# Performance work log

Measured on AMD Instinct MI355X. Metric: run time of the kernel, lower is better.

Reference implementation:

```python
import jax, jax.numpy as jnp
import numpy as np

N, E, T, D, M, G = 131072, 524288, 4, 128, 256, 4096
VOCAB, GH, L, PASSES = 100, 512, 128, 4


def setup_inputs() -> dict:
    key = jax.random.key(0)
    ks = jax.random.split(key, 20)
    node_types = jax.random.randint(ks[0], (N,), 0, VOCAB)
    edge_src = jax.random.randint(ks[1], (E,), 0, N)
    edge_dst = jax.random.randint(ks[2], (E,), 0, N)
    edge_type = jax.random.randint(ks[3], (E,), 0, T)
    inner = jnp.sort(jax.random.randint(ks[4], (G - 1,), 0, N))
    ptr = jnp.concatenate([jnp.zeros((1,), jnp.int64 if inner.dtype == jnp.int64 else jnp.int32),
                           inner, jnp.full((1,), N, inner.dtype)])
    s = 1.0 / np.sqrt(D)
    emb = jax.random.normal(ks[5], (VOCAB, D), jnp.float32)
    W_msg = jax.random.normal(ks[6], (T, M, D), jnp.float32) * s
    b_msg = jax.random.normal(ks[7], (T, M), jnp.float32) * s
    W_ih = jax.random.normal(ks[8], (3 * D, M), jnp.float32) * (1.0 / np.sqrt(M))
    W_hh = jax.random.normal(ks[9], (3 * D, D), jnp.float32) * s
    b_ih = jax.random.normal(ks[10], (3 * D,), jnp.float32) * s
    b_hh = jax.random.normal(ks[11], (3 * D,), jnp.float32) * s
    W_gate = jax.random.normal(ks[12], (1, D), jnp.float32) * s
    b_gate = jax.random.normal(ks[13], (1,), jnp.float32) * s
    W_n2g = jax.random.normal(ks[14], (GH, D), jnp.float32) * s
    b_n2g = jax.random.normal(ks[15], (GH,), jnp.float32) * s
    W_loc = jax.random.normal(ks[16], (L, GH), jnp.float32) * (1.0 / np.sqrt(GH))
    b_loc = jax.random.normal(ks[17], (L,), jnp.float32) * (1.0 / np.sqrt(GH))
    W_lv = jax.random.normal(ks[18], (L, GH), jnp.float32) * (1.0 / np.sqrt(GH))
    b_lv = jax.random.normal(ks[19], (L,), jnp.float32) * (1.0 / np.sqrt(GH))
    return dict(node_types=node_types, edge_src=edge_src, edge_dst=edge_dst,
                edge_type=edge_type, ptr=ptr, emb=emb, W_msg=W_msg, b_msg=b_msg,
                W_ih=W_ih, W_hh=W_hh, b_ih=b_ih, b_hh=b_hh, W_gate=W_gate,
                b_gate=b_gate, W_n2g=W_n2g, b_n2g=b_n2g, W_loc=W_loc, b_loc=b_loc,
                W_lv=W_lv, b_lv=b_lv)


def _ggnn_pass(h, edge_src, edge_dst, edge_type, W_msg, b_msg, W_ih, W_hh, b_ih, b_hh):
    # per-edge-type linear on all nodes: [T, N, M]
    msgs_all = jnp.einsum('nd,tmd->tnm', h, W_msg) + b_msg[:, None, :]
    # gather the message of the edge's type at its source node: [E, M]
    e_msg = msgs_all[edge_type, edge_src]
    # sparse adjacency matmul == scatter-add of source messages into destinations
    agg = jax.ops.segment_sum(e_msg, edge_dst, num_segments=h.shape[0])
    m = jax.nn.relu(agg)
    # torch GRUCell
    gi = m @ W_ih.T + b_ih      # [N, 3D]
    gh = h @ W_hh.T + b_hh      # [N, 3D]
    d = h.shape[1]
    ir, iz, inn = gi[:, :d], gi[:, d:2 * d], gi[:, 2 * d:]
    hr, hz, hn = gh[:, :d], gh[:, d:2 * d], gh[:, 2 * d:]
    r = jax.nn.sigmoid(ir + hr)
    z = jax.nn.sigmoid(iz + hz)
    n = jnp.tanh(inn + r * hn)
    return (1.0 - z) * n + z * h


def reference(node_types, edge_src, edge_dst, edge_type, ptr, emb, W_msg, b_msg,
              W_ih, W_hh, b_ih, b_hh, W_gate, b_gate, W_n2g, b_n2g,
              W_loc, b_loc, W_lv, b_lv):
    h = emb[node_types]  # [N, D]
    for _ in range(PASSES):
        h = _ggnn_pass(h, edge_src, edge_dst, edge_type,
                       W_msg, b_msg, W_ih, W_hh, b_ih, b_hh)
    # gated segment readout (equivalent to per-graph attn @ h slices)
    gate = jax.nn.sigmoid(h @ W_gate.T + b_gate)        # [N, 1]
    hg = h @ W_n2g.T + b_n2g                            # [N, GH]
    seg = jnp.searchsorted(ptr, jnp.arange(h.shape[0]), side='right') - 1
    h_graph = jax.ops.segment_sum(gate * hg, seg, num_segments=ptr.shape[0] - 1)
    z_loc = h_graph @ W_loc.T + b_loc
    z_logvar = h_graph @ W_lv.T + b_lv
    return (z_loc, z_logvar)
```

## Files before the change

### kernel.cpp

```cpp
#include <hip/hip_runtime.h>
#include <cstdint>
#include <cstddef>

#define NN 131072
#define EE 524288
#define GG 4096
#define NPASS 4

typedef __attribute__((ext_vector_type(4))) float f32x4;
typedef __attribute__((ext_vector_type(8))) short bfrag;

__device__ __forceinline__ unsigned short f2bf(float f) {
  union { float f; unsigned u; } v; v.f = f;
  unsigned r = v.u + 0x7fffu + ((v.u >> 16) & 1u);
  return (unsigned short)(r >> 16);
}
__device__ __forceinline__ float bf2f(unsigned short h) {
  union { unsigned u; float f; } v; v.u = ((unsigned)h) << 16;
  return v.f;
}
__device__ __forceinline__ unsigned pack2(float x, float y) {
  return (unsigned)f2bf(x) | ((unsigned)f2bf(y) << 16);
}
__device__ __forceinline__ float sigm(float x) { return 1.f / (1.f + __expf(-x)); }

__device__ __forceinline__ void cp16(unsigned short* l, const unsigned short* g) {
  __builtin_amdgcn_global_load_lds(
      (const __attribute__((address_space(1))) unsigned int*)g,
      (__attribute__((address_space(3))) unsigned int*)l, 16, 0, 0);
}

__global__ void prep_wb(const float* __restrict__ Wmsg, unsigned short* __restrict__ Wb) {
  int idx = blockIdx.x * 256 + threadIdx.x;
  if (idx >= 256 * 512) return;
  int m = idx >> 9, k = idx & 511;
  int t = k >> 7, d = k & 127;
  Wb[idx] = f2bf(Wmsg[((size_t)t * 256 + m) * 128 + d]);
}

__global__ void prep_wgru(const float* __restrict__ Wih, const float* __restrict__ Whh,
                          unsigned short* __restrict__ Wgru) {
  int idx = blockIdx.x * 256 + threadIdx.x;
  if (idx >= 512 * 384) return;
  int j = idx / 384, kk = idx % 384;
  float v;
  if (kk < 256) v = (j < 384) ? Wih[j * 256 + kk] : 0.f;
  else          v = (j < 256) ? Whh[j * 128 + (kk - 256)]
                   : ((j >= 384) ? Whh[(j - 128) * 128 + (kk - 256)] : 0.f);
  int g = (j < 128) ? 0 : (j < 256) ? 1 : (j < 384) ? 2 : 3;
  int d = j & 127;
  Wgru[(size_t)(4 * d + g) * 384 + kk] = f2bf(v);
}

__global__ void prep_bias(const float* __restrict__ bih, const float* __restrict__ bhh,
                          float* __restrict__ biasg) {
  int j = blockIdx.x * 256 + threadIdx.x;
  if (j >= 512) return;
  float v;
  if (j < 256) v = bih[j] + bhh[j];
  else if (j < 384) v = bih[j];
  else v = bhh[j - 128];
  int g = (j < 128) ? 0 : (j < 256) ? 1 : (j < 384) ? 2 : 3;
  int d = j & 127;
  biasg[4 * d + g] = v;
}

__global__ void compose_k(const float* __restrict__ Wloc, const float* __restrict__ Wlv,
                          const float* __restrict__ Wn2g, float* __restrict__ WcT) {
  int b = blockIdx.x;
  int jl = threadIdx.x >> 7, d = threadIdx.x & 127;
  int j = b * 2 + jl;
  const float* wx = (j < 128) ? Wloc + (size_t)j * 512 : Wlv + (size_t)(j - 128) * 512;
  float acc = 0.f;
  for (int k = 0; k < 512; k++) acc += wx[k] * Wn2g[k * 128 + d];
  WcT[d * 256 + j] = acc;
}

__global__ void cvec_k(const float* __restrict__ Wloc, const float* __restrict__ Wlv,
                       const float* __restrict__ bn2g, float* __restrict__ cvec) {
  int j = threadIdx.x;
  const float* wx = (j < 128) ? Wloc + (size_t)j * 512 : Wlv + (size_t)(j - 128) * 512;
  float a = 0.f;
  for (int k = 0; k < 512; k++) a += wx[k] * bn2g[k];
  cvec[j] = a;
}

__global__ void init_h(const int* __restrict__ nt, const float* __restrict__ emb,
                       unsigned short* __restrict__ H) {
  size_t idx = (size_t)blockIdx.x * 256 + threadIdx.x;
  int n = (int)(idx >> 7), d = (int)(idx & 127);
  H[idx] = f2bf(emb[(size_t)nt[n] * 128 + d]);
}

__global__ void cnt4_k(const int* __restrict__ edst, const int* __restrict__ etype,
                       int* __restrict__ cnti) {
  int e = blockIdx.x * 256 + threadIdx.x;
  if (e >= EE) return;
  atomicAdd(&cnti[edst[e] * 4 + etype[e]], 1);
}

__global__ void degsum_k(const int* __restrict__ cnti, int* __restrict__ deg,
                         float* __restrict__ cnt) {
  int n = blockIdx.x * 256 + threadIdx.x;
  if (n >= NN) return;
  int4 c4 = *(const int4*)&cnti[n * 4];
  deg[n] = c4.x + c4.y + c4.z + c4.w;
  float4 f4 = make_float4((float)c4.x, (float)c4.y, (float)c4.z, (float)c4.w);
  *(float4*)&cnt[n * 4] = f4;
}

__global__ __launch_bounds__(1024) void scan_k(const int* __restrict__ deg,
                                               int* __restrict__ rowptr,
                                               int* __restrict__ cursor) {
  __shared__ int part[1024];
  int t = threadIdx.x;
  int base = t * 128;
  int s = 0;
  for (int i = 0; i < 128; i++) s += deg[base + i];
  part[t] = s;
  __syncthreads();
  for (int off = 1; off < 1024; off <<= 1) {
    int v = (t >= off) ? part[t - off] : 0;
    __syncthreads();
    part[t] += v;
    __syncthreads();
  }
  int run = part[t] - s;
  for (int i = 0; i < 128; i++) {
    rowptr[base + i] = run;
    cursor[base + i] = run;
    run += deg[base + i];
  }
  if (t == 1023) rowptr[NN] = run;
}

__global__ void fill_k(const int* __restrict__ esrc, const int* __restrict__ edst,
                       const int* __restrict__ etype, int* __restrict__ cursor,
                       unsigned* __restrict__ epack) {
  int e = blockIdx.x * 256 + threadIdx.x;
  if (e >= EE) return;
  int pos = atomicAdd(&cursor[edst[e]], 1);
  epack[pos] = ((unsigned)etype[e] << 17) | (unsigned)esrc[e];
}

__global__ __launch_bounds__(256) void agg_k(const int* __restrict__ rowptr,
                                             const unsigned* __restrict__ epack,
                                             const unsigned short* __restrict__ H,
                                             unsigned short* __restrict__ s) {
  int n = blockIdx.x * 4 + (threadIdx.x >> 6);
  int lane = threadIdx.x & 63;
  int beg = rowptr[n], end = rowptr[n + 1];
  const unsigned short* hbase = H + lane * 2;
  float a0 = 0.f, a1 = 0.f, b0 = 0.f, b1 = 0.f;
  float c0 = 0.f, c1 = 0.f, d0 = 0.f, d1 = 0.f;
#define ACCUM(P, HV)                                              \
  {                                                               \
    int t_ = (int)((P) >> 17);                                    \
    float v0_ = bf2f((unsigned short)((HV) & 0xffffu));           \
    float v1_ = bf2f((unsigned short)((HV) >> 16));               \
    if (t_ == 0)      { a0 += v0_; a1 += v1_; }                   \
    else if (t_ == 1) { b0 += v0_; b1 += v1_; }                   \
    else if (t_ == 2) { c0 += v0_; c1 += v1_; }                   \
    else              { d0 += v0_; d1 += v1_; }                   \
  }
  for (int base = beg; base < end; base += 64) {
    int cnt = end - base;
    if (cnt > 64) cnt = 64;
    int mye = base + lane;
    unsigned ep = (mye < end) ? epack[mye] : 0u;
    if (cnt > 0) {
      unsigned p = (unsigned)__shfl((int)ep, 0);
      unsigned hv = *(const unsigned*)&hbase[(size_t)(p & 0x1FFFFu) * 128];
      for (int j = 1; j < cnt; j++) {
        unsigned pn = (unsigned)__shfl((int)ep, j);
        unsigned hvn = *(const unsigned*)&hbase[(size_t)(pn & 0x1FFFFu) * 128];
        ACCUM(p, hv);
        p = pn;
        hv = hvn;
      }
      ACCUM(p, hv);
    }
  }
#undef ACCUM
  unsigned short* srow = s + (size_t)n * 512;
  *(unsigned*)&srow[0 * 128 + lane * 2] = pack2(a0, a1);
  *(unsigned*)&srow[1 * 128 + lane * 2] = pack2(b0, b1);
  *(unsigned*)&srow[2 * 128 + lane * 2] = pack2(c0, c1);
  *(unsigned*)&srow[3 * 128 + lane * 2] = pack2(d0, d1);
}

__global__ __launch_bounds__(256, 4) void msgemm_k(
    unsigned short* __restrict__ s, const float* __restrict__ cnt,
    const unsigned short* __restrict__ Wb, const float* __restrict__ bmsg) {
  __shared__ __align__(16) unsigned short As[2][64 * 32];
  __shared__ __align__(16) unsigned short Bs[2][256 * 32];
  int i0 = blockIdx.x * 64;
  int tid = threadIdx.x, lane = tid & 63, w = tid >> 6;
  int wi = w >> 1, wj = w & 1;
  int q = lane >> 4, r = lane & 15;
  int srow = tid >> 2, scol = (tid & 3) * 8;

  const unsigned short* sP = s + (size_t)(i0 + srow) * 512 + scol;
  const unsigned short* WbP = Wb + (size_t)srow * 512 + scol;

  f32x4 acc[2][8];
#pragma unroll
  for (int a = 0; a < 2; a++)
#pragma unroll
    for (int b = 0; b < 8; b++) acc[a][b] = f32x4{0.f, 0.f, 0.f, 0.f};

  cp16(&As[0][w * 512], sP);
#pragma unroll
  for (int c = 0; c < 4; c++)
    cp16(&Bs[0][c * 2048 + w * 512], WbP + (size_t)(c * 64) * 512);
  __syncthreads();

  for (int ks = 0; ks < 16; ks++) {
    int b = ks & 1;
    if (ks < 15) {
      int nb = b ^ 1;
      cp16(&As[nb][w * 512], sP + (ks + 1) * 32);
#pragma unroll
      for (int c = 0; c < 4; c++)
        cp16(&Bs[nb][c * 2048 + w * 512],
             WbP + (size_t)(c * 64) * 512 + (ks + 1) * 32);
    }
    bfrag af[2];
#pragma unroll
    for (int rt = 0; rt < 2; rt++)
      af[rt] = *(const bfrag*)&As[b][(wi * 32 + rt * 16 + r) * 32 + q * 8];
#pragma unroll
    for (int ct = 0; ct < 8; ct++) {
      bfrag bfr = *(const bfrag*)&Bs[b][(wj * 128 + ct * 16 + r) * 32 + q * 8];
#pragma unroll
      for (int rt = 0; rt < 2; rt++)
        acc[rt][ct] =
            __builtin_amdgcn_mfma_f32_16x16x32_bf16(af[rt], bfr, acc[rt][ct], 0, 0, 0);
    }
    __syncthreads();
  }

#pragma unroll
  for (int ct = 0; ct < 8; ct++) {
    int j = wj * 128 + ct * 16 + r;
    float b0 = bmsg[j], b1 = bmsg[256 + j], b2 = bmsg[512 + j], b3 = bmsg[768 + j];
#pragma unroll
    for (int rt = 0; rt < 2; rt++) {
#pragma unroll
      for (int reg = 0; reg < 4; reg++) {
        int il = wi * 32 + rt * 16 + q * 4 + reg;
        float4 c4 = *(const float4*)&cnt[(size_t)(i0 + il) * 4];
        float v = acc[rt][ct][reg] + c4.x * b0 + c4.y * b1 + c4.z * b2 + c4.w * b3;
        v = v > 0.f ? v : 0.f;
        s[(size_t)(i0 + il) * 512 + j] = f2bf(v);
      }
    }
  }
}

__global__ __launch_bounds__(256, 4) void grugemm_k(
    const unsigned short* __restrict__ m,
    const unsigned short* __restrict__ Hc, unsigned short* __restrict__ Hn,
    const unsigned short* __restrict__ Wgru, const float* __restrict__ biasg) {
  __shared__ __align__(16) unsigned short As[2][64 * 32];
  __shared__ __align__(16) unsigned short Bs[2][256 * 32];
  int bcol = blockIdx.x & 1;
  int i0 = (int)(blockIdx.x >> 1) * 64;
  int tid = threadIdx.x, lane = tid & 63, w = tid >> 6;
  int wi = w >> 1, wj = w & 1;
  int q = lane >> 4, r = lane & 15;
  int srow = tid >> 2, scol = (tid & 3) * 8;

  const unsigned short* mP = m + (size_t)(i0 + srow) * 512 + scol;
  const unsigned short* hP = Hc + (size_t)(i0 + srow) * 128 + scol;
  const unsigned short* WgP = Wgru + (size_t)(bcol * 256 + srow) * 384 + scol;

  f32x4 acc[2][8];
#pragma unroll
  for (int a = 0; a < 2; a++)
#pragma unroll
    for (int b = 0; b < 8; b++) acc[a][b] = f32x4{0.f, 0.f, 0.f, 0.f};

  cp16(&As[0][w * 512], mP);
#pragma unroll
  for (int c = 0; c < 4; c++)
    cp16(&Bs[0][c * 2048 + w * 512], WgP + (size_t)(c * 64) * 384);
  __syncthreads();

  for (int ks = 0; ks < 12; ks++) {
    int b = ks & 1;
    if (ks < 11) {
      int nb = b ^ 1;
      int nks = ks + 1;
      const unsigned short* aSrc =
          (nks < 8) ? (mP + nks * 32) : (hP + (nks - 8) * 32);
      cp16(&As[nb][w * 512], aSrc);
#pragma unroll
      for (int c = 0; c < 4; c++)
        cp16(&Bs[nb][c * 2048 + w * 512],
             WgP + (size_t)(c * 64) * 384 + nks * 32);
    }
    bfrag af[2];
#pragma unroll
    for (int rt = 0; rt < 2; rt++)
      af[rt] = *(const bfrag*)&As[b][(wi * 32 + rt * 16 + r) * 32 + q * 8];
#pragma unroll
    for (int ct = 0; ct < 8; ct++) {
      bfrag bfr = *(const bfrag*)&Bs[b][(wj * 128 + ct * 16 + r) * 32 + q * 8];
#pragma unroll
      for (int rt = 0; rt < 2; rt++)
        acc[rt][ct] =
            __builtin_amdgcn_mfma_f32_16x16x32_bf16(af[rt], bfr, acc[rt][ct], 0, 0, 0);
    }
    __syncthreads();
  }

  int rr = r & 3;
  bool s1 = (lane & 1) != 0, s2 = (lane & 2) != 0;
#pragma unroll
  for (int ct = 0; ct < 8; ct++) {
    float bias = biasg[bcol * 256 + wj * 128 + ct * 16 + r];
    int d = bcol * 64 + wj * 32 + ct * 4 + (r >> 2);
#pragma unroll
    for (int rt = 0; rt < 2; rt++) {
      float v0 = acc[rt][ct][0] + bias;
      float v1 = acc[rt][ct][1] + bias;
      float v2 = acc[rt][ct][2] + bias;
      float v3 = acc[rt][ct][3] + bias;
      float t, rcv;
      t = s1 ? v0 : v1; rcv = __shfl_xor(t, 1);
      v0 = s1 ? rcv : v0; v1 = s1 ? v1 : rcv;
      t = s1 ? v2 : v3; rcv = __shfl_xor(t, 1);
      v2 = s1 ? rcv : v2; v3 = s1 ? v3 : rcv;
      t = s2 ? v0 : v2; rcv = __shfl_xor(t, 2);
      v0 = s2 ? rcv : v0; v2 = s2 ? v2 : rcv;
      t = s2 ? v1 : v3; rcv = __shfl_xor(t, 2);
      v1 = s2 ? rcv : v1; v3 = s2 ? v3 : rcv;
      int i = i0 + wi * 32 + rt * 16 + q * 4 + rr;
      size_t hoff = (size_t)i * 128 + d;
      float hold = bf2f(Hc[hoff]);
      float rg = sigm(v0), zg = sigm(v1);
      float ng = tanhf(v2 + rg * v3);
      Hn[hoff] = f2bf((1.f - zg) * ng + zg * hold);
    }
  }
}

__global__ __launch_bounds__(256) void gate_k(const unsigned short* __restrict__ H,
                                              const float* __restrict__ Wg,
                                              const float* __restrict__ bg,
                                              float* __restrict__ gate) {
  __shared__ float wg[128];
  if (threadIdx.x < 128) wg[threadIdx.x] = Wg[threadIdx.x];
  __syncthreads();
  int g = threadIdx.x >> 4, sub = threadIdx.x & 15;
  int n = blockIdx.x * 16 + g;
  const unsigned short* hr = H + (size_t)n * 128;
  float p = 0.f;
  for (int k = sub; k < 128; k += 16) p += bf2f(hr[k]) * wg[k];
  p += __shfl_xor(p, 1);
  p += __shfl_xor(p, 2);
  p += __shfl_xor(p, 4);
  p += __shfl_xor(p, 8);
  if (sub == 0) gate[n] = sigm(p + bg[0]);
}

__global__ __launch_bounds__(256) void gsum_k(const unsigned short* __restrict__ H,
                                              const float* __restrict__ gate,
                                              const int* __restrict__ ptr,
                                              float* __restrict__ gsum,
                                              float* __restrict__ sg) {
  int g = blockIdx.x * 4 + (threadIdx.x >> 6);
  int lane = threadIdx.x & 63;
  int start = ptr[g], end = ptr[g + 1];
  float a0 = 0.f, a1 = 0.f, gs = 0.f;
  for (int n = start; n < end; n++) {
    float gt = gate[n];
    unsigned hv = *(const unsigned*)&H[(size_t)n * 128 + lane * 2];
    a0 += gt * bf2f((unsigned short)(hv & 0xffffu));
    a1 += gt * bf2f((unsigned short)(hv >> 16));
    gs += gt;
  }
  gsum[(size_t)g * 128 + lane * 2] = a0;
  gsum[(size_t)g * 128 + lane * 2 + 1] = a1;
  if (lane == 0) sg[g] = gs;
}

__global__ __launch_bounds__(256) void zfinal_k(const float* __restrict__ gsum,
                                                const float* __restrict__ sg,
                                                const float* __restrict__ WcT,
                                                const float* __restrict__ cvec,
                                                const float* __restrict__ bloc,
                                                const float* __restrict__ blv,
                                                float* __restrict__ out) {
  __shared__ float gs[128];
  __shared__ float sgs;
  int g = blockIdx.x;
  int j = threadIdx.x;
  if (j < 128) gs[j] = gsum[(size_t)g * 128 + j];
  if (j == 0) sgs = sg[g];
  __syncthreads();
  float acc = (j < 128 ? bloc[j] : blv[j - 128]) + sgs * cvec[j];
  for (int d = 0; d < 128; d++) acc += gs[d] * WcT[d * 256 + j];
  size_t o = (j < 128) ? ((size_t)g * 128 + j)
                       : ((size_t)GG * 128 + (size_t)g * 128 + (j - 128));
  out[o] = acc;
}

extern "C" void kernel_launch(void* const* d_in, const int* in_sizes, int n_in,
                              void* d_out, int out_size, void* d_ws, size_t ws_size,
                              hipStream_t stream) {
  const int* node_types = (const int*)d_in[0];
  const int* esrc = (const int*)d_in[1];
  const int* edst = (const int*)d_in[2];
  const int* etype = (const int*)d_in[3];
  const int* ptr = (const int*)d_in[4];
  const float* emb = (const float*)d_in[5];
  const float* Wmsg = (const float*)d_in[6];
  const float* bmsg = (const float*)d_in[7];
  const float* Wih = (const float*)d_in[8];
  const float* Whh = (const float*)d_in[9];
  const float* bih = (const float*)d_in[10];
  const float* bhh = (const float*)d_in[11];
  const float* Wg = (const float*)d_in[12];
  const float* bg = (const float*)d_in[13];
  const float* Wn2g = (const float*)d_in[14];
  const float* bn2g = (const float*)d_in[15];
  const float* Wloc = (const float*)d_in[16];
  const float* bloc = (const float*)d_in[17];
  const float* Wlv = (const float*)d_in[18];
  const float* blv = (const float*)d_in[19];
  float* out = (float*)d_out;

  char* ws = (char*)d_ws;
  size_t off = 0;
  unsigned short* s = (unsigned short*)(ws);
  off += (size_t)NN * 512 * 2;
  unsigned short* H0 = (unsigned short*)(ws + off);
  off += (size_t)NN * 128 * 2;
  unsigned short* H1 = (unsigned short*)(ws + off);
  off += (size_t)NN * 128 * 2;
  float* cnt = (float*)(ws + off);
  off += (size_t)NN * 4 * 4;
  int* cnti = (int*)(ws + off);
  off += (size_t)NN * 4 * 4;
  int* deg = (int*)(ws + off);
  off += (size_t)NN * 4;
  int* rowptr = (int*)(ws + off);
  off += (size_t)(NN + 64) * 4;
  int* cursor = (int*)(ws + off);
  off += (size_t)NN * 4;
  unsigned* epack = (unsigned*)(ws + off);
  off += (size_t)EE * 4;
  float* gate = (float*)(ws + off);
  off += (size_t)NN * 4;
  float* gsum = (float*)(ws + off);
  off += (size_t)GG * 128 * 4;
  float* sg = (float*)(ws + off);
  off += (size_t)GG * 4;
  float* WcT = (float*)(ws + off);
  off += 128 * 256 * 4;
  float* cvec = (float*)(ws + off);
  off += 256 * 4;
  unsigned short* Wb = (unsigned short*)(ws + off);
  off += 256 * 512 * 2;
  unsigned short* Wgru = (unsigned short*)(ws + off);
  off += 512 * 384 * 2;
  float* biasg = (float*)(ws + off);
  off += 512 * 4;

  hipMemsetAsync(cnti, 0, (size_t)NN * 16, stream);
  prep_wb<<<512, 256, 0, stream>>>(Wmsg, Wb);
  prep_wgru<<<768, 256, 0, stream>>>(Wih, Whh, Wgru);
  prep_bias<<<2, 256, 0, stream>>>(bih, bhh, biasg);
  compose_k<<<128, 256, 0, stream>>>(Wloc, Wlv, Wn2g, WcT);
  cvec_k<<<1, 256, 0, stream>>>(Wloc, Wlv, bn2g, cvec);
  init_h<<<NN * 128 / 256, 256, 0, stream>>>(node_types, emb, H0);
  cnt4_k<<<EE / 256, 256, 0, stream>>>(edst, etype, cnti);
  degsum_k<<<NN / 256, 256, 0, stream>>>(cnti, deg, cnt);
  scan_k<<<1, 1024, 0, stream>>>(deg, rowptr, cursor);
  fill_k<<<EE / 256, 256, 0, stream>>>(esrc, edst, etype, cursor, epack);

  unsigned short* Hc = H0;
  unsigned short* Hn = H1;
  for (int p = 0; p < NPASS; p++) {
    agg_k<<<NN / 4, 256, 0, stream>>>(rowptr, epack, Hc, s);
    msgemm_k<<<NN / 64, 256, 0, stream>>>(s, cnt, Wb, bmsg);
    grugemm_k<<<NN / 64 * 2, 256, 0, stream>>>(s, Hc, Hn, Wgru, biasg);
    unsigned short* tmp = Hc; Hc = Hn; Hn = tmp;
  }

  gate_k<<<NN / 16, 256, 0, stream>>>(Hc, Wg, bg, gate);
  gsum_k<<<GG / 4, 256, 0, stream>>>(Hc, gate, ptr, gsum, sg);
  zfinal_k<<<GG, 256, 0, stream>>>(gsum, sg, WcT, cvec, bloc, blv, out);
}
```

Before: 1.312 ms.

## Enlarge GEMM tiles to 128 rows with 512 threads, swizzle LDS, remap blocks

New measurement: 1.192 ms. -9.2%, faster.

```diff
diff --git a/kernel.cpp b/kernel.cpp
--- a/kernel.cpp
+++ b/kernel.cpp
@@ -189,19 +189,32 @@
   *(unsigned*)&srow[3 * 128 + lane * 2] = pack2(d0, d1);
 }
 
-__global__ __launch_bounds__(256, 4) void msgemm_k(
+__global__ __launch_bounds__(512, 4) void msgemm_k(
     unsigned short* __restrict__ s, const float* __restrict__ cnt,
     const unsigned short* __restrict__ Wb, const float* __restrict__ bmsg) {
-  __shared__ __align__(16) unsigned short As[2][64 * 32];
+  __shared__ __align__(16) unsigned short As[2][128 * 32];
   __shared__ __align__(16) unsigned short Bs[2][256 * 32];
-  int i0 = blockIdx.x * 64;
+  int i0 = blockIdx.x * 128;
   int tid = threadIdx.x, lane = tid & 63, w = tid >> 6;
   int wi = w >> 1, wj = w & 1;
   int q = lane >> 4, r = lane & 15;
-  int srow = tid >> 2, scol = (tid & 3) * 8;
-
-  const unsigned short* sP = s + (size_t)(i0 + srow) * 512 + scol;
-  const unsigned short* WbP = Wb + (size_t)srow * 512 + scol;
+  int srow = tid >> 2;
+  int swcol = ((tid & 3) ^ ((srow >> 1) & 3)) * 8;
+
+  const unsigned short* sP = s + (size_t)(i0 + srow) * 512 + swcol;
+  const unsigned short* WbP = Wb + (size_t)srow * 512 + swcol;
+
+  int aoff[2], boff[8];
+#pragma unroll
+  for (int rt = 0; rt < 2; rt++) {
+    int row = wi * 32 + rt * 16 + r;
+    aoff[rt] = row * 32 + (q ^ ((row >> 1) & 3)) * 8;
+  }
+#pragma unroll
+  for (int ct = 0; ct < 8; ct++) {
+    int row = wj * 128 + ct * 16 + r;
+    boff[ct] = row * 32 + (q ^ ((row >> 1) & 3)) * 8;
+  }
 
   f32x4 acc[2][8];
 #pragma unroll
@@ -211,8 +224,8 @@
 
   cp16(&As[0][w * 512], sP);
 #pragma unroll
-  for (int c = 0; c < 4; c++)
-    cp16(&Bs[0][c * 2048 + w * 512], WbP + (size_t)(c * 64) * 512);
+  for (int c = 0; c < 2; c++)
+    cp16(&Bs[0][c * 4096 + w * 512], WbP + (size_t)(c * 128) * 512);
   __syncthreads();
 
   for (int ks = 0; ks < 16; ks++) {
@@ -221,17 +234,16 @@
       int nb = b ^ 1;
       cp16(&As[nb][w * 512], sP + (ks + 1) * 32);
 #pragma unroll
-      for (int c = 0; c < 4; c++)
-        cp16(&Bs[nb][c * 2048 + w * 512],
-             WbP + (size_t)(c * 64) * 512 + (ks + 1) * 32);
+      for (int c = 0; c < 2; c++)
+        cp16(&Bs[nb][c * 4096 + w * 512],
+             WbP + (size_t)(c * 128) * 512 + (ks + 1) * 32);
     }
     bfrag af[2];
 #pragma unroll
-    for (int rt = 0; rt < 2; rt++)
-      af[rt] = *(const bfrag*)&As[b][(wi * 32 + rt * 16 + r) * 32 + q * 8];
+    for (int rt = 0; rt < 2; rt++) af[rt] = *(const bfrag*)&As[b][aoff[rt]];
 #pragma unroll
     for (int ct = 0; ct < 8; ct++) {
-      bfrag bfr = *(const bfrag*)&Bs[b][(wj * 128 + ct * 16 + r) * 32 + q * 8];
+      bfrag bfr = *(const bfrag*)&Bs[b][boff[ct]];
 #pragma unroll
       for (int rt = 0; rt < 2; rt++)
         acc[rt][ct] =
@@ -258,22 +270,36 @@
   }
 }
 
-__global__ __launch_bounds__(256, 4) void grugemm_k(
+__global__ __launch_bounds__(512, 4) void grugemm_k(
     const unsigned short* __restrict__ m,
     const unsigned short* __restrict__ Hc, unsigned short* __restrict__ Hn,
     const unsigned short* __restrict__ Wgru, const float* __restrict__ biasg) {
-  __shared__ __align__(16) unsigned short As[2][64 * 32];
+  __shared__ __align__(16) unsigned short As[2][128 * 32];
   __shared__ __align__(16) unsigned short Bs[2][256 * 32];
-  int bcol = blockIdx.x & 1;
-  int i0 = (int)(blockIdx.x >> 1) * 64;
+  int wg = (blockIdx.x & 7) * 256 + (blockIdx.x >> 3);
+  int bcol = wg & 1;
+  int i0 = (wg >> 1) * 128;
   int tid = threadIdx.x, lane = tid & 63, w = tid >> 6;
   int wi = w >> 1, wj = w & 1;
   int q = lane >> 4, r = lane & 15;
-  int srow = tid >> 2, scol = (tid & 3) * 8;
-
-  const unsigned short* mP = m + (size_t)(i0 + srow) * 512 + scol;
-  const unsigned short* hP = Hc + (size_t)(i0 + srow) * 128 + scol;
-  const unsigned short* WgP = Wgru + (size_t)(bcol * 256 + srow) * 384 + scol;
+  int srow = tid >> 2;
+  int swcol = ((tid & 3) ^ ((srow >> 1) & 3)) * 8;
+
+  const unsigned short* mP = m + (size_t)(i0 + srow) * 512 + swcol;
+  const unsigned short* hP = Hc + (size_t)(i0 + srow) * 128 + swcol;
+  const unsigned short* WgP = Wgru + (size_t)(bcol * 256 + srow) * 384 + swcol;
+
+  int aoff[2], boff[8];
+#pragma unroll
+  for (int rt = 0; rt < 2; rt++) {
+    int row = wi * 32 + rt * 16 + r;
+    aoff[rt] = row * 32 + (q ^ ((row >> 1) & 3)) * 8;
+  }
+#pragma unroll
+  for (int ct = 0; ct < 8; ct++) {
+    int row = wj * 128 + ct * 16 + r;
+    boff[ct] = row * 32 + (q ^ ((row >> 1) & 3)) * 8;
+  }
 
   f32x4 acc[2][8];
 #pragma unroll
@@ -283,8 +309,8 @@
 
   cp16(&As[0][w * 512], mP);
 #pragma unroll
-  for (int c = 0; c < 4; c++)
-    cp16(&Bs[0][c * 2048 + w * 512], WgP + (size_t)(c * 64) * 384);
+  for (int c = 0; c < 2; c++)
+    cp16(&Bs[0][c * 4096 + w * 512], WgP + (size_t)(c * 128) * 384);
   __syncthreads();
 
   for (int ks = 0; ks < 12; ks++) {
@@ -296,17 +322,16 @@
           (nks < 8) ? (mP + nks * 32) : (hP + (nks - 8) * 32);
       cp16(&As[nb][w * 512], aSrc);
 #pragma unroll
-      for (int c = 0; c < 4; c++)
-        cp16(&Bs[nb][c * 2048 + w * 512],
-             WgP + (size_t)(c * 64) * 384 + nks * 32);
+      for (int c = 0; c < 2; c++)
+        cp16(&Bs[nb][c * 4096 + w * 512],
+             WgP + (size_t)(c * 128) * 384 + nks * 32);
     }
     bfrag af[2];
 #pragma unroll
-    for (int rt = 0; rt < 2; rt++)
-      af[rt] = *(const bfrag*)&As[b][(wi * 32 + rt * 16 + r) * 32 + q * 8];
+    for (int rt = 0; rt < 2; rt++) af[rt] = *(const bfrag*)&As[b][aoff[rt]];
 #pragma unroll
     for (int ct = 0; ct < 8; ct++) {
-      bfrag bfr = *(const bfrag*)&Bs[b][(wj * 128 + ct * 16 + r) * 32 + q * 8];
+      bfrag bfr = *(const bfrag*)&Bs[b][boff[ct]];
 #pragma unroll
       for (int rt = 0; rt < 2; rt++)
         acc[rt][ct] =
@@ -485,8 +510,8 @@
   unsigned short* Hn = H1;
   for (int p = 0; p < NPASS; p++) {
     agg_k<<<NN / 4, 256, 0, stream>>>(rowptr, epack, Hc, s);
-    msgemm_k<<<NN / 64, 256, 0, stream>>>(s, cnt, Wb, bmsg);
-    grugemm_k<<<NN / 64 * 2, 256, 0, stream>>>(s, Hc, Hn, Wgru, biasg);
+    msgemm_k<<<NN / 128, 512, 0, stream>>>(s, cnt, Wb, bmsg);
+    grugemm_k<<<NN / 128 * 2, 512, 0, stream>>>(s, Hc, Hn, Wgru, biasg);
     unsigned short* tmp = Hc; Hc = Hn; Hn = tmp;
   }
 
```
